# Performance work log

Measured on AMD Instinct MI355X. Metric: run time of the kernel, lower is better.

Reference implementation:

```python
import jax, jax.numpy as jnp
import numpy as np

COMMITMENT_COST = 0.25


def setup_inputs() -> dict:
    key = jax.random.key(0)
    k1, k2 = jax.random.split(key)
    inputs = jax.random.normal(k1, (64, 2048, 64), dtype=jnp.float32)   # [B, T, D]
    embedding = jax.random.normal(k2, (512, 64), dtype=jnp.float32)     # [K, D] codebook
    return {"inputs": inputs, "embedding": embedding}


def reference(inputs, embedding):
    B, T, D = inputs.shape
    K = embedding.shape[0]
    flat = inputs.reshape(-1, D)                                        # [N, D]
    distances = (jnp.sum(flat * flat, axis=1, keepdims=True)
                 + jnp.sum(embedding * embedding, axis=1)
                 - 2.0 * jnp.matmul(flat, embedding.T))
    idx = jnp.argmin(distances, axis=1)                                 # [N]
    # gather-based quantization (same math as one-hot @ codebook)
    quantized = jnp.take(embedding, idx, axis=0).reshape(inputs.shape)  # [B, T, D]
    e_latent_loss = jnp.mean((jax.lax.stop_gradient(quantized) - inputs) ** 2)
    vq_loss = COMMITMENT_COST * e_latent_loss
    # straight-through estimator
    quantized_st = inputs + jax.lax.stop_gradient(quantized - inputs)
    # perplexity from code-usage histogram (scatter-add instead of dense one-hot)
    N = flat.shape[0]
    avg_probs = jnp.zeros((K,), dtype=flat.dtype).at[idx].add(1.0) / N
    perplexity = jnp.exp(-jnp.sum(avg_probs * jnp.log(avg_probs + 1e-10)))
    enc_indices = idx.reshape(B, T)
    return quantized_st, vq_loss, perplexity, enc_indices
```

## Files before the change

### kernel.cpp

```cpp
#include <hip/hip_runtime.h>

#define NROWS 131072
#define D 64
#define K 512
#define TPB 512
#define RPB 512
#define NBLK (NROWS/RPB)

#define LOSS_OFF (NROWS*D)
#define PERP_OFF (LOSS_OFF+1)
#define IDX_OFF  (LOSS_OFF+2)

typedef _Float16 h16x8 __attribute__((ext_vector_type(8)));
typedef float    f32x4 __attribute__((ext_vector_type(4)));


__device__ __forceinline__ void split8_f16(float4 a, float4 b,
                                           h16x8* h8, h16x8* m8)
{
    float xf[8] = {a.x,a.y,a.z,a.w,b.x,b.y,b.z,b.w};
    _Float16 hh[8], mm[8];
    #pragma unroll
    for (int j = 0; j < 8; ++j) {
        float v = xf[j];
        _Float16 h = (_Float16)v;
        float hf = (float)h;
        if (fabsf(hf) < 6.1035156e-5f) { h = (_Float16)0.f; hf = 0.f; }
        hh[j] = h;
        mm[j] = (_Float16)((v - hf) * 4096.f);
    }
    *h8 = (h16x8){hh[0],hh[1],hh[2],hh[3],hh[4],hh[5],hh[6],hh[7]};
    *m8 = (h16x8){mm[0],mm[1],mm[2],mm[3],mm[4],mm[5],mm[6],mm[7]};
}

__global__ __launch_bounds__(64) void vq_prep(
    const float* __restrict__ emb, float* __restrict__ e2, h16x8* __restrict__ bfrag)
{
    const int ct = blockIdx.x, l = threadIdx.x;
    const int q = l >> 4, r16 = l & 15;
    const int code = ct*16 + r16;
    const float4* e4 = reinterpret_cast<const float4*>(emb + (size_t)code * D);
    #pragma unroll
    for (int s = 0; s < 2; ++s) {
        float4 f0 = e4[q*2 + s*8];
        float4 f1 = e4[q*2 + s*8 + 1];
        float4 g0 = {-2.f*f0.x, -2.f*f0.y, -2.f*f0.z, -2.f*f0.w};
        float4 g1 = {-2.f*f1.x, -2.f*f1.y, -2.f*f1.z, -2.f*f1.w};
        h16x8 g, n;
        split8_f16(g0, g1, &g, &n);
        bfrag[(ct*4 + 0 + s)*64 + l] = g;
        bfrag[(ct*4 + 2 + s)*64 + l] = n;
    }
    if (l < 16) {
        const float* e = emb + (size_t)(ct*16 + l) * D;
        float s0=0.f,s1=0.f,s2=0.f,s3=0.f;
        #pragma unroll
        for (int d = 0; d < D; d += 4) {
            s0 = fmaf(e[d+0], e[d+0], s0);
            s1 = fmaf(e[d+1], e[d+1], s1);
            s2 = fmaf(e[d+2], e[d+2], s2);
            s3 = fmaf(e[d+3], e[d+3], s3);
        }
        e2[ct*16 + l] = (s0+s1)+(s2+s3);
    }
}

#define MFMA_(AV, BV, CI) __builtin_amdgcn_mfma_f32_16x16x32_f16((AV), (BV), (CI), 0, 0, 0)

#define LOADB(B0,B1,B2,B3,E2V, CT) do {                             \
    const h16x8* _bp = sBl + (size_t)(CT)*4*64;                     \
    B0 = _bp[0*64]; B1 = _bp[1*64];                                 \
    B2 = _bp[2*64]; B3 = _bp[3*64];                                 \
    E2V = se2[((CT) << 4) + r16];                                   \
} while (0)

#define TILE_MFMA_ALL(B0,B1,B2,B3, E2V) do {                                      \
    f32x4 _ci = {(E2V),(E2V),(E2V),(E2V)};                                        \
    __builtin_amdgcn_s_setprio(1);                                                \
    _Pragma("unroll") for (int mt=0; mt<4; ++mt) SA[mt] = MFMA_(Ah[mt][0], B0, _ci);     \
    _Pragma("unroll") for (int mt=0; mt<4; ++mt) SB[mt] = MFMA_(Ah[mt][0], B2, zero4);   \
    _Pragma("unroll") for (int mt=0; mt<4; ++mt) SA[mt] = MFMA_(Ah[mt][1], B1, SA[mt]);  \
    _Pragma("unroll") for (int mt=0; mt<4; ++mt) SB[mt] = MFMA_(Am[mt][0], B0, SB[mt]);  \
    _Pragma("unroll") for (int mt=0; mt<4; ++mt) SB[mt] = MFMA_(Ah[mt][1], B3, SB[mt]);  \
    _Pragma("unroll") for (int mt=0; mt<4; ++mt) SB[mt] = MFMA_(Am[mt][1], B1, SB[mt]);  \
    __builtin_amdgcn_s_setprio(0);                                                \
} while (0)

#define TILE_ARGMIN_ALL(CT) do {                                             \
    const int _col = ((CT) << 4) + r16;                                      \
    _Pragma("unroll")                                                        \
    for (int mt = 0; mt < 4; ++mt)                                           \
        _Pragma("unroll")                                                    \
        for (int g = 0; g < 4; ++g) {                                        \
            float dst = fmaf(SB[mt][g], 2.44140625e-4f, SA[mt][g]);          \
            if (dst < bestd[mt][g]) { bestd[mt][g] = dst; besti[mt][g] = _col; } \
        }                                                                    \
} while (0)

__global__ __launch_bounds__(TPB, 1) void vq_main(
    const float* __restrict__ x, const float* __restrict__ emb,
    const float* __restrict__ e2g, const h16x8* __restrict__ bfrag,
    float* __restrict__ out, float* __restrict__ wsum, int* __restrict__ whist)
{
    __shared__ h16x8 sB[32*4*64];
    __shared__ float se2[K];
    __shared__ int   shist[K];
    __shared__ int   sidx[RPB];

    const int t = threadIdx.x;
    for (int i = t; i < K; i += TPB) { shist[i] = 0; se2[i] = e2g[i]; }
    for (int i = t; i < 32*4*64; i += TPB) sB[i] = bfrag[i];
    __syncthreads();

    const int l = t & 63, w = t >> 6;
    const int q = l >> 4, r16 = l & 15;
    const int wbase = w * 64;
    const h16x8* sBl = sB + l;
    const f32x4 zero4 = {0.f,0.f,0.f,0.f};
    const float4* x4 = reinterpret_cast<const float4*>(x);
    const int rowpanel = blockIdx.x * RPB;

    h16x8 Ah[4][2], Am[4][2];
    #pragma unroll
    for (int mt = 0; mt < 4; ++mt) {
        #pragma unroll
        for (int s = 0; s < 2; ++s) {
            int rl = rowpanel + wbase + mt*16 + r16;
            float4 f0 = x4[(size_t)rl*16 + q*2 + s*8];
            float4 f1 = x4[(size_t)rl*16 + q*2 + s*8 + 1];
            split8_f16(f0, f1, &Ah[mt][s], &Am[mt][s]);
        }
    }

    float bestd[4][4];
    int   besti[4][4];
    #pragma unroll
    for (int mt = 0; mt < 4; ++mt)
        #pragma unroll
        for (int g = 0; g < 4; ++g) { bestd[mt][g] = 3.4e38f; besti[mt][g] = 0; }

    f32x4 SA[4], SB[4];

    h16x8 p0,p1,p2,p3; float pe2;
    h16x8 q0,q1,q2,q3; float qe2;
    LOADB(p0,p1,p2,p3,pe2, 0);
    LOADB(q0,q1,q2,q3,qe2, 1);

    #pragma clang loop unroll(disable)
    for (int ct = 0; ct < 32; ct += 2) {
        TILE_MFMA_ALL(p0,p1,p2,p3, pe2);
        LOADB(p0,p1,p2,p3,pe2, (ct + 2) & 31);
        TILE_ARGMIN_ALL(ct);
        TILE_MFMA_ALL(q0,q1,q2,q3, qe2);
        LOADB(q0,q1,q2,q3,qe2, (ct + 3) & 31);
        TILE_ARGMIN_ALL(ct + 1);
    }

    #pragma unroll
    for (int mask = 1; mask <= 8; mask <<= 1) {
        #pragma unroll
        for (int mt = 0; mt < 4; ++mt)
            #pragma unroll
            for (int g = 0; g < 4; ++g) {
                float od = __shfl_xor(bestd[mt][g], mask, 64);
                int   oi = __shfl_xor(besti[mt][g], mask, 64);
                if (od < bestd[mt][g] ||
                    (od == bestd[mt][g] && oi < besti[mt][g])) {
                    bestd[mt][g] = od; besti[mt][g] = oi;
                }
            }
    }
    if (r16 == 0) {
        #pragma unroll
        for (int mt = 0; mt < 4; ++mt)
            #pragma unroll
            for (int g = 0; g < 4; ++g)
                sidx[wbase + mt*16 + q*4 + g] = besti[mt][g];
    }
    __syncthreads();

    const int row = t;
    const int grow = rowpanel + row;
    const int bi = sidx[row];
    float dsum = 0.f;
    {
        const float4* eq = reinterpret_cast<const float4*>(emb + (size_t)bi * D);
        const float4* xg = x4 + (size_t)grow*16;
        float4* o = reinterpret_cast<float4*>(out + (size_t)grow * D);
        #pragma unroll
        for (int i = 0; i < 16; ++i) {
            float4 xv = xg[i];
            float4 qv = eq[i];
            float4 v;
            float d0,d1,d2,d3;
            d0 = qv.x - xv.x; v.x = xv.x + d0; dsum = fmaf(d0,d0,dsum);
            d1 = qv.y - xv.y; v.y = xv.y + d1; dsum = fmaf(d1,d1,dsum);
            d2 = qv.z - xv.z; v.z = xv.z + d2; dsum = fmaf(d2,d2,dsum);
            d3 = qv.w - xv.w; v.w = xv.w + d3; dsum = fmaf(d3,d3,dsum);
            o[i] = v;
        }
    }
    out[IDX_OFF + grow] = (float)bi;
    atomicAdd(&shist[bi], 1);

    #pragma unroll
    for (int off = 32; off > 0; off >>= 1)
        dsum += __shfl_xor(dsum, off, 64);
    if ((t & 63) == 0)
        atomicAdd(wsum, dsum);

    __syncthreads();
    for (int i = t; i < K; i += TPB)
        if (shist[i]) atomicAdd(&whist[i], shist[i]);
}

__global__ __launch_bounds__(K) void vq_finalize(
    const float* __restrict__ wsum, const int* __restrict__ whist,
    float* __restrict__ out)
{
    __shared__ float red[K];
    int t = threadIdx.x;
    float c = (float)whist[t];
    float p = c / (float)NROWS;
    red[t] = p * logf(p + 1e-10f);
    __syncthreads();
    for (int s = K/2; s > 0; s >>= 1) {
        if (t < s) red[t] += red[t+s];
        __syncthreads();
    }
    if (t == 0) {
        out[PERP_OFF] = expf(-red[0]);
        out[LOSS_OFF] = 0.25f * (wsum[0] / (float)(NROWS*D));
    }
}

extern "C" void kernel_launch(void* const* d_in, const int* in_sizes, int n_in,
                              void* d_out, int out_size, void* d_ws, size_t ws_size,
                              hipStream_t stream)
{
    const float* x   = (const float*)d_in[0];
    const float* emb = (const float*)d_in[1];
    float* out   = (float*)d_out;
    float* wsum  = (float*)d_ws;
    int*   whist = (int*)((char*)d_ws + 256);
    float* e2    = (float*)((char*)d_ws + 4096);
    h16x8* bfrag = (h16x8*)((char*)d_ws + 8192);

    hipMemsetAsync(d_ws, 0, 4096, stream);
    vq_prep<<<32, 64, 0, stream>>>(emb, e2, bfrag);
    vq_main<<<NBLK, TPB, 0, stream>>>(x, emb, e2, bfrag, out, wsum, whist);
    vq_finalize<<<1, K, 0, stream>>>(wsum, whist, out);
}
```

Measured before the change: 81.45 us.

## Shrink row panel per block and read codebook fragments from global memory

```diff
diff --git a/kernel.cpp b/kernel.cpp
--- a/kernel.cpp
+++ b/kernel.cpp
@@ -3,8 +3,8 @@
 #define NROWS 131072
 #define D 64
 #define K 512
-#define TPB 512
-#define RPB 512
+#define TPB 256
+#define RPB 64
 #define NBLK (NROWS/RPB)
 
 #define LOSS_OFF (NROWS*D)
@@ -68,33 +68,27 @@
 #define MFMA_(AV, BV, CI) __builtin_amdgcn_mfma_f32_16x16x32_f16((AV), (BV), (CI), 0, 0, 0)
 
 #define LOADB(B0,B1,B2,B3,E2V, CT) do {                             \
-    const h16x8* _bp = sBl + (size_t)(CT)*4*64;                     \
+    const h16x8* _bp = bbase + (size_t)(CT)*4*64;                   \
     B0 = _bp[0*64]; B1 = _bp[1*64];                                 \
     B2 = _bp[2*64]; B3 = _bp[3*64];                                 \
-    E2V = se2[((CT) << 4) + r16];                                   \
+    E2V = e2g[((CT) << 4) + r16];                                   \
 } while (0)
 
-#define TILE_MFMA_ALL(B0,B1,B2,B3, E2V) do {                                      \
-    f32x4 _ci = {(E2V),(E2V),(E2V),(E2V)};                                        \
-    __builtin_amdgcn_s_setprio(1);                                                \
-    _Pragma("unroll") for (int mt=0; mt<4; ++mt) SA[mt] = MFMA_(Ah[mt][0], B0, _ci);     \
-    _Pragma("unroll") for (int mt=0; mt<4; ++mt) SB[mt] = MFMA_(Ah[mt][0], B2, zero4);   \
-    _Pragma("unroll") for (int mt=0; mt<4; ++mt) SA[mt] = MFMA_(Ah[mt][1], B1, SA[mt]);  \
-    _Pragma("unroll") for (int mt=0; mt<4; ++mt) SB[mt] = MFMA_(Am[mt][0], B0, SB[mt]);  \
-    _Pragma("unroll") for (int mt=0; mt<4; ++mt) SB[mt] = MFMA_(Ah[mt][1], B3, SB[mt]);  \
-    _Pragma("unroll") for (int mt=0; mt<4; ++mt) SB[mt] = MFMA_(Am[mt][1], B1, SB[mt]);  \
-    __builtin_amdgcn_s_setprio(0);                                                \
-} while (0)
-
-#define TILE_ARGMIN_ALL(CT) do {                                             \
-    const int _col = ((CT) << 4) + r16;                                      \
-    _Pragma("unroll")                                                        \
-    for (int mt = 0; mt < 4; ++mt)                                           \
-        _Pragma("unroll")                                                    \
-        for (int g = 0; g < 4; ++g) {                                        \
-            float dst = fmaf(SB[mt][g], 2.44140625e-4f, SA[mt][g]);          \
-            if (dst < bestd[mt][g]) { bestd[mt][g] = dst; besti[mt][g] = _col; } \
-        }                                                                    \
+#define UNIT(B0,B1,B2,B3,E2V, CT) do {                              \
+    f32x4 _ci = {(E2V),(E2V),(E2V),(E2V)};                          \
+    f32x4 SA, SB;                                                   \
+    SA = MFMA_(Ah[0], B0, _ci);                                     \
+    SB = MFMA_(Ah[0], B2, zero4);                                   \
+    SA = MFMA_(Ah[1], B1, SA);                                      \
+    SB = MFMA_(Am[0], B0, SB);                                      \
+    SB = MFMA_(Ah[1], B3, SB);                                      \
+    SB = MFMA_(Am[1], B1, SB);                                      \
+    const int _col = ((CT) << 4) + r16;                             \
+    _Pragma("unroll")                                               \
+    for (int g = 0; g < 4; ++g) {                                   \
+        float dst = fmaf(SB[g], 2.44140625e-4f, SA[g]);             \
+        if (dst < bestd[g]) { bestd[g] = dst; besti[g] = _col; }    \
+    }                                                               \
 } while (0)
 
 __global__ __launch_bounds__(TPB, 1) void vq_main(
@@ -102,44 +96,34 @@
     const float* __restrict__ e2g, const h16x8* __restrict__ bfrag,
     float* __restrict__ out, float* __restrict__ wsum, int* __restrict__ whist)
 {
-    __shared__ h16x8 sB[32*4*64];
-    __shared__ float se2[K];
     __shared__ int   shist[K];
     __shared__ int   sidx[RPB];
+    __shared__ float sred[4];
 
     const int t = threadIdx.x;
-    for (int i = t; i < K; i += TPB) { shist[i] = 0; se2[i] = e2g[i]; }
-    for (int i = t; i < 32*4*64; i += TPB) sB[i] = bfrag[i];
-    __syncthreads();
+    for (int i = t; i < K; i += TPB) shist[i] = 0;
 
     const int l = t & 63, w = t >> 6;
     const int q = l >> 4, r16 = l & 15;
-    const int wbase = w * 64;
-    const h16x8* sBl = sB + l;
+    const float4* x4 = reinterpret_cast<const float4*>(x);
+    const int rowbase = blockIdx.x * RPB + w * 16;
+
+    h16x8 Ah[2], Am[2];
+    #pragma unroll
+    for (int s = 0; s < 2; ++s) {
+        int rl = rowbase + r16;
+        float4 f0 = x4[(size_t)rl*16 + q*2 + s*8];
+        float4 f1 = x4[(size_t)rl*16 + q*2 + s*8 + 1];
+        split8_f16(f0, f1, &Ah[s], &Am[s]);
+    }
+
+    float bestd[4];
+    int   besti[4];
+    #pragma unroll
+    for (int g = 0; g < 4; ++g) { bestd[g] = 3.4e38f; besti[g] = 0; }
+
+    const h16x8* bbase = bfrag + l;
     const f32x4 zero4 = {0.f,0.f,0.f,0.f};
-    const float4* x4 = reinterpret_cast<const float4*>(x);
-    const int rowpanel = blockIdx.x * RPB;
-
-    h16x8 Ah[4][2], Am[4][2];
-    #pragma unroll
-    for (int mt = 0; mt < 4; ++mt) {
-        #pragma unroll
-        for (int s = 0; s < 2; ++s) {
-            int rl = rowpanel + wbase + mt*16 + r16;
-            float4 f0 = x4[(size_t)rl*16 + q*2 + s*8];
-            float4 f1 = x4[(size_t)rl*16 + q*2 + s*8 + 1];
-            split8_f16(f0, f1, &Ah[mt][s], &Am[mt][s]);
-        }
-    }
-
-    float bestd[4][4];
-    int   besti[4][4];
-    #pragma unroll
-    for (int mt = 0; mt < 4; ++mt)
-        #pragma unroll
-        for (int g = 0; g < 4; ++g) { bestd[mt][g] = 3.4e38f; besti[mt][g] = 0; }
-
-    f32x4 SA[4], SB[4];
 
     h16x8 p0,p1,p2,p3; float pe2;
     h16x8 q0,q1,q2,q3; float qe2;
@@ -148,47 +132,41 @@
 
     #pragma clang loop unroll(disable)
     for (int ct = 0; ct < 32; ct += 2) {
-        TILE_MFMA_ALL(p0,p1,p2,p3, pe2);
+        UNIT(p0,p1,p2,p3,pe2, ct);
         LOADB(p0,p1,p2,p3,pe2, (ct + 2) & 31);
-        TILE_ARGMIN_ALL(ct);
-        TILE_MFMA_ALL(q0,q1,q2,q3, qe2);
+        UNIT(q0,q1,q2,q3,qe2, ct + 1);
         LOADB(q0,q1,q2,q3,qe2, (ct + 3) & 31);
-        TILE_ARGMIN_ALL(ct + 1);
     }
 
     #pragma unroll
     for (int mask = 1; mask <= 8; mask <<= 1) {
         #pragma unroll
-        for (int mt = 0; mt < 4; ++mt)
-            #pragma unroll
-            for (int g = 0; g < 4; ++g) {
-                float od = __shfl_xor(bestd[mt][g], mask, 64);
-                int   oi = __shfl_xor(besti[mt][g], mask, 64);
-                if (od < bestd[mt][g] ||
-                    (od == bestd[mt][g] && oi < besti[mt][g])) {
-                    bestd[mt][g] = od; besti[mt][g] = oi;
-                }
+        for (int g = 0; g < 4; ++g) {
+            float od = __shfl_xor(bestd[g], mask, 64);
+            int   oi = __shfl_xor(besti[g], mask, 64);
+            if (od < bestd[g] ||
+                (od == bestd[g] && oi < besti[g])) {
+                bestd[g] = od; besti[g] = oi;
             }
+        }
     }
     if (r16 == 0) {
         #pragma unroll
-        for (int mt = 0; mt < 4; ++mt)
-            #pragma unroll
-            for (int g = 0; g < 4; ++g)
-                sidx[wbase + mt*16 + q*4 + g] = besti[mt][g];
+        for (int g = 0; g < 4; ++g)
+            sidx[w*16 + q*4 + g] = besti[g];
     }
     __syncthreads();
 
-    const int row = t;
-    const int grow = rowpanel + row;
+    const int row = t >> 2, part = t & 3;
+    const int grow = blockIdx.x * RPB + row;
     const int bi = sidx[row];
     float dsum = 0.f;
     {
-        const float4* eq = reinterpret_cast<const float4*>(emb + (size_t)bi * D);
-        const float4* xg = x4 + (size_t)grow*16;
-        float4* o = reinterpret_cast<float4*>(out + (size_t)grow * D);
-        #pragma unroll
-        for (int i = 0; i < 16; ++i) {
+        const float4* eq = reinterpret_cast<const float4*>(emb + (size_t)bi * D) + part*4;
+        const float4* xg = x4 + (size_t)grow*16 + part*4;
+        float4* o = reinterpret_cast<float4*>(out + (size_t)grow * D) + part*4;
+        #pragma unroll
+        for (int i = 0; i < 4; ++i) {
             float4 xv = xg[i];
             float4 qv = eq[i];
             float4 v;
@@ -200,16 +178,19 @@
             o[i] = v;
         }
     }
-    out[IDX_OFF + grow] = (float)bi;
-    atomicAdd(&shist[bi], 1);
+    if (part == 0) {
+        out[IDX_OFF + grow] = (float)bi;
+        atomicAdd(&shist[bi], 1);
+    }
 
     #pragma unroll
     for (int off = 32; off > 0; off >>= 1)
         dsum += __shfl_xor(dsum, off, 64);
-    if ((t & 63) == 0)
-        atomicAdd(wsum, dsum);
-
+    if (l == 0) sred[w] = dsum;
     __syncthreads();
+    if (t == 0)
+        atomicAdd(wsum, (sred[0] + sred[1]) + (sred[2] + sred[3]));
+
     for (int i = t; i < K; i += TPB)
         if (shist[i]) atomicAdd(&whist[i], shist[i]);
 }
```

After: 77.38 us. -5.0%, faster.
